# Performance work log

Hardware: AMD Instinct MI355X
Metric: run time of the kernel (lower is better)

Reference implementation:

```python
import jax, jax.numpy as jnp
import numpy as np

N_NODES = 100000
N_EDGES = 1000000
IN_CH = 128
HID = 128


def setup_inputs() -> dict:
    key = jax.random.key(0)
    ks = jax.random.split(key, 8)
    node_features = jax.random.normal(ks[0], (N_NODES, IN_CH), dtype=jnp.float32)
    edge_index = jax.random.randint(ks[1], (2, N_EDGES), 0, N_NODES, dtype=jnp.int64)
    # Linear params (PyTorch convention: W [out,in], y = x @ W.T + b), Kaiming-ish scale
    Wdim = jax.random.normal(ks[2], (HID, IN_CH), dtype=jnp.float32) / np.sqrt(IN_CH)
    bdim = jnp.zeros((HID,), dtype=jnp.float32)
    W1 = jax.random.normal(ks[3], (HID, 2 * HID), dtype=jnp.float32) / np.sqrt(2 * HID)
    b1 = jnp.zeros((HID,), dtype=jnp.float32)
    W2 = jax.random.normal(ks[4], (1, HID), dtype=jnp.float32) / np.sqrt(HID)
    b2 = jnp.zeros((1,), dtype=jnp.float32)
    return {"node_features": node_features, "edge_index": edge_index,
            "Wdim": Wdim, "bdim": bdim, "W1": W1, "b1": b1, "W2": W2, "b2": b2}


def reference(node_features, edge_index, Wdim, bdim, W1, b1, W2, b2):
    # gather endpoint features [E, in_ch]
    src = node_features[edge_index[0]]
    dst = node_features[edge_index[1]]
    # shared first projection + ReLU (dropout = identity at eval)
    x = jax.nn.relu(src @ Wdim.T + bdim)  # [E, H]
    y = jax.nn.relu(dst @ Wdim.T + bdim)  # [E, H]
    # elementwise combine -> [E, 2H]
    edge_feat = jnp.concatenate([x * y, x - y], axis=1)
    h = jax.nn.relu(edge_feat @ W1.T + b1)  # [E, H]
    prob = jax.nn.sigmoid(h @ W2.T + b2)  # [E, 1]
    return prob
```

## Files before the change

### kernel.cpp

```cpp
#include <hip/hip_runtime.h>
#include <hip/hip_bf16.h>


#define N_NODES 100000
#define N_EDGES 1000000
#define NT      31250
#define GRID    1024

typedef unsigned int u32;
typedef u32   u32x2 __attribute__((ext_vector_type(2)));
typedef u32   u32x4 __attribute__((ext_vector_type(4)));
typedef float f32x4 __attribute__((ext_vector_type(4)));
typedef float f32x16 __attribute__((ext_vector_type(16)));
typedef __bf16 bf16x8 __attribute__((ext_vector_type(8)));
typedef _Float16 f16x8 __attribute__((ext_vector_type(8)));

__device__ inline u32 pack2bf(float a, float b) {
    unsigned short ua = __builtin_bit_cast(unsigned short, (__bf16)a);
    unsigned short ub = __builtin_bit_cast(unsigned short, (__bf16)b);
    return (u32)ua | ((u32)ub << 16);
}
__device__ inline u32 pack2h(float a, float b) {
    unsigned short ua = __builtin_bit_cast(unsigned short, (_Float16)a);
    unsigned short ub = __builtin_bit_cast(unsigned short, (_Float16)b);
    return (u32)ua | ((u32)ub << 16);
}

__device__ __forceinline__ void gload16(const unsigned char* g, unsigned char* l) {
    __builtin_amdgcn_global_load_lds(
        (__attribute__((address_space(1))) unsigned int*)g,
        (__attribute__((address_space(3))) unsigned int*)l,
        16, 0, 0);
}

__global__ __launch_bounds__(256, 1) void k_project(
    const float* __restrict__ nf, const float* __restrict__ Wdim,
    const float* __restrict__ bdim, unsigned short* __restrict__ P)
{
    __shared__ unsigned char lA[128 * 256];
    const int t = threadIdx.x;
    for (int ci = t; ci < 2048; ci += 256) {
        const int row = ci >> 4;
        const int k8 = (ci & 15) << 3;
        const float* wp = Wdim + (row << 7) + k8;
        f32x4 v0 = *(const f32x4*)wp;
        f32x4 v1 = *(const f32x4*)(wp + 4);
        u32x4 pk = { pack2bf(v0[0], v0[1]), pack2bf(v0[2], v0[3]),
                     pack2bf(v1[0], v1[1]), pack2bf(v1[2], v1[3]) };
        int byte = (row << 8) + (k8 << 1);
        byte ^= (row & 15) << 4;
        *(u32x4*)(lA + byte) = pk;
    }
    __syncthreads();

    const int lane = t & 63;
    const int wave = t >> 6;
    const int cc = lane & 31;
    const int h  = lane >> 5;
    const int tile = blockIdx.x * 4 + wave;
    if (tile >= 3125) return;
    const int node = (tile << 5) + cc;
    const float* xrow = nf + ((size_t)node << 7);

    f32x4 rv[16];
#pragma unroll
    for (int kt = 0; kt < 8; ++kt) {
        const int kf = (kt << 4) + (h << 3);
        rv[2*kt]   = *(const f32x4*)(xrow + kf);
        rv[2*kt+1] = *(const f32x4*)(xrow + kf + 4);
    }

    f32x16 acc[4] = {};
#pragma unroll
    for (int kt = 0; kt < 8; ++kt) {
        const int kf = (kt << 4) + (h << 3);
        f32x4 v0 = rv[2*kt], v1 = rv[2*kt+1];
        bf16x8 bf;
        bf[0]=(__bf16)v0[0]; bf[1]=(__bf16)v0[1]; bf[2]=(__bf16)v0[2]; bf[3]=(__bf16)v0[3];
        bf[4]=(__bf16)v1[0]; bf[5]=(__bf16)v1[1]; bf[6]=(__bf16)v1[2]; bf[7]=(__bf16)v1[3];
        const int off = kf << 1;
#pragma unroll
        for (int t4 = 0; t4 < 4; ++t4) {
            const int arow = (t4 << 5) + cc;
            const int ab = ((arow << 8) + off) ^ ((arow & 15) << 4);
            bf16x8 af = __builtin_bit_cast(bf16x8, *(const u32x4*)(lA + ab));
            acc[t4] = __builtin_amdgcn_mfma_f32_32x32x16_bf16(af, bf, acc[t4], 0, 0, 0);
        }
    }
    unsigned short* prow = P + ((size_t)node << 7);
#pragma unroll
    for (int t4 = 0; t4 < 4; ++t4) {
#pragma unroll
        for (int q = 0; q < 4; ++q) {
            const int chb = (t4 << 5) + (q << 3) + (h << 2);
            f32x4 bb = *(const f32x4*)(bdim + chb);
            const float h0 = fmaxf(acc[t4][(q << 2) + 0] + bb[0], 0.f);
            const float h1 = fmaxf(acc[t4][(q << 2) + 1] + bb[1], 0.f);
            const float h2 = fmaxf(acc[t4][(q << 2) + 2] + bb[2], 0.f);
            const float h3 = fmaxf(acc[t4][(q << 2) + 3] + bb[3], 0.f);
            u32x2 st = { pack2h(h0, h1), pack2h(h2, h3) };
            *(u32x2*)(prow + chb) = st;
        }
    }
}

__global__ __launch_bounds__(256, 2) void k_edge(
    const unsigned short* __restrict__ P,
    const int* __restrict__ ei,
    const float* __restrict__ W1, const float* __restrict__ b1,
    const float* __restrict__ W2, const float* __restrict__ b2,
    float* __restrict__ out)
{
    __shared__ unsigned char buf[2][64 * 256];
    __shared__ float pr[2][4][32];
    __shared__ float sb1[128], sw2[128];
    const int t = threadIdx.x;
    const int lane = t & 63;
    const int wave = t >> 6;
    const int cc = lane & 31;
    const int h  = lane >> 5;
    if (t < 128) { sb1[t] = b1[t]; sw2[t] = W2[t]; }

    f16x8 wf[16];
    {
        const float* wrow = W1 + (((wave << 5) + cc) << 8);
#pragma unroll
        for (int kt = 0; kt < 8; ++kt) {
#pragma unroll
            for (int half = 0; half < 2; ++half) {
                const float* wp = wrow + (half << 7) + (kt << 4) + (h << 3);
                f32x4 a = *(const f32x4*)wp;
                f32x4 b = *(const f32x4*)(wp + 4);
                f16x8 f;
                f[0]=(_Float16)a[0]; f[1]=(_Float16)a[1]; f[2]=(_Float16)a[2]; f[3]=(_Float16)a[3];
                f[4]=(_Float16)b[0]; f[5]=(_Float16)b[1]; f[6]=(_Float16)b[2]; f[7]=(_Float16)b[3];
                wf[(kt << 1) + half] = f;
            }
        }
    }

    const unsigned char* Pb = (const unsigned char*)P;
    const int* eb = ei + (wave < 2 ? 0 : N_EDGES - 32);
    int xo[4], rbase[4];
#pragma unroll
    for (int i = 0; i < 4; ++i) {
        const int rl = (i << 2) + (lane >> 4);
        xo[i] = ((lane & 15) ^ (rl & 15)) << 4;
        rbase[i] = (wave << 4) + rl;
    }
    const float b2v = b2[0];
    const int t0 = blockIdx.x;

    int nidx0, nidx1, nidx2, nidx3;
    {
        int i0 = eb[(t0 << 5) + rbase[0]];
        int i1 = eb[(t0 << 5) + rbase[1]];
        int i2 = eb[(t0 << 5) + rbase[2]];
        int i3 = eb[(t0 << 5) + rbase[3]];
        gload16(Pb + ((size_t)i0 << 8) + xo[0], &buf[0][(rbase[0] & ~3) << 8]);
        gload16(Pb + ((size_t)i1 << 8) + xo[1], &buf[0][(rbase[1] & ~3) << 8]);
        gload16(Pb + ((size_t)i2 << 8) + xo[2], &buf[0][(rbase[2] & ~3) << 8]);
        gload16(Pb + ((size_t)i3 << 8) + xo[3], &buf[0][(rbase[3] & ~3) << 8]);
        int tn = t0 + GRID; tn = tn < NT ? tn : NT - 1;
        nidx0 = eb[(tn << 5) + rbase[0]];
        nidx1 = eb[(tn << 5) + rbase[1]];
        nidx2 = eb[(tn << 5) + rbase[2]];
        nidx3 = eb[(tn << 5) + rbase[3]];
    }
    __syncthreads();

    int p = 0;
    for (int tl = t0; tl < NT; tl += GRID) {
        unsigned char* nb = buf[p ^ 1];
        gload16(Pb + ((size_t)nidx0 << 8) + xo[0], nb + ((rbase[0] & ~3) << 8));
        gload16(Pb + ((size_t)nidx1 << 8) + xo[1], nb + ((rbase[1] & ~3) << 8));
        gload16(Pb + ((size_t)nidx2 << 8) + xo[2], nb + ((rbase[2] & ~3) << 8));
        gload16(Pb + ((size_t)nidx3 << 8) + xo[3], nb + ((rbase[3] & ~3) << 8));
        {
            int tn = tl + 2 * GRID; tn = tn < NT ? tn : NT - 1;
            nidx0 = eb[(tn << 5) + rbase[0]];
            nidx1 = eb[(tn << 5) + rbase[1]];
            nidx2 = eb[(tn << 5) + rbase[2]];
            nidx3 = eb[(tn << 5) + rbase[3]];
        }

        const unsigned char* bp_ = buf[p];
        const unsigned char* xb = bp_ + (cc << 8);
        const unsigned char* yb = bp_ + ((32 + cc) << 8);
        const int cx = cc & 15;
        f32x16 acc = {};
#pragma unroll
        for (int kt = 0; kt < 8; ++kt) {
            const int co = (((kt << 1) + h) ^ cx) << 4;
            const f16x8 xh = __builtin_bit_cast(f16x8, *(const u32x4*)(xb + co));
            const f16x8 yh = __builtin_bit_cast(f16x8, *(const u32x4*)(yb + co));
            const f16x8 bp = xh * yh;
            const f16x8 bd = xh - yh;
            acc = __builtin_amdgcn_mfma_f32_32x32x16_f16(wf[(kt << 1) + 0], bp, acc, 0, 0, 0);
            acc = __builtin_amdgcn_mfma_f32_32x32x16_f16(wf[(kt << 1) + 1], bd, acc, 0, 0, 0);
        }

        float partial = 0.f;
#pragma unroll
        for (int q = 0; q < 4; ++q) {
            const int chb = (wave << 5) + (q << 3) + (h << 2);
            const f32x4 bb = *(const f32x4*)(sb1 + chb);
            const f32x4 ww = *(const f32x4*)(sw2 + chb);
#pragma unroll
            for (int rr = 0; rr < 4; ++rr) {
                const float hv = fmaxf(acc[(q << 2) + rr] + bb[rr], 0.f);
                partial += hv * ww[rr];
            }
        }
        partial += __shfl_xor(partial, 32);
        if (h == 0) pr[p][wave][cc] = partial;

        __syncthreads();

        if (t < 32) {
            const float z = pr[p][0][t] + pr[p][1][t] + pr[p][2][t] + pr[p][3][t] + b2v;
            out[(tl << 5) + t] = 1.0f / (1.0f + __expf(-z));
        }
        p ^= 1;
    }
}

extern "C" void kernel_launch(void* const* d_in, const int* in_sizes, int n_in,
                              void* d_out, int out_size, void* d_ws, size_t ws_size,
                              hipStream_t stream) {
    const float* nf   = (const float*)d_in[0];
    const int*   ei   = (const int*)d_in[1];
    const float* Wdim = (const float*)d_in[2];
    const float* bdim = (const float*)d_in[3];
    const float* W1   = (const float*)d_in[4];
    const float* b1   = (const float*)d_in[5];
    const float* W2   = (const float*)d_in[6];
    const float* b2   = (const float*)d_in[7];
    float* out = (float*)d_out;
    unsigned short* P = (unsigned short*)d_ws;

    k_project<<<dim3(782), dim3(256), 0, stream>>>(nf, Wdim, bdim, P);
    k_edge<<<dim3(GRID), dim3(256), 0, stream>>>(P, ei, W1, b1, W2, b2, out);
}
```

Baseline: 150.6 us.

## Triple-buffer edge gathers with explicit waitcnt and deferred output writes

Replaces the double-buffered LDS gather pipeline in the edge kernel with a three-stage ring of buffers, prefetching gathered node rows two tiles ahead. A manual s_waitcnt vmcnt plus s_barrier replaces __syncthreads, and each tile's sigmoid output is written in the following iteration, which removes one barrier per tile. The grid drops from 1024 to 768 blocks to fit the extra LDS buffer. The intent is to hide gather latency better, at the cost of more LDS per block and reliance on hand-counted vmcnt values, which could be fragile.

```diff
diff --git a/kernel.cpp b/kernel.cpp
--- a/kernel.cpp
+++ b/kernel.cpp
@@ -5,7 +5,7 @@
 #define N_NODES 100000
 #define N_EDGES 1000000
 #define NT      31250
-#define GRID    1024
+#define GRID    768
 
 typedef unsigned int u32;
 typedef u32   u32x2 __attribute__((ext_vector_type(2)));
@@ -107,11 +107,13 @@
 __global__ __launch_bounds__(256, 2) void k_edge(
     const unsigned short* __restrict__ P,
     const int* __restrict__ ei,
-    const float* __restrict__ W1, const float* __restrict__ b1,
-    const float* __restrict__ W2, const float* __restrict__ b2,
+    const float* __restrict__ W1, const float* __restrict__ B1,
+    const float* __restrict__ W2, const float* __restrict__ B2,
     float* __restrict__ out)
 {
-    __shared__ unsigned char buf[2][64 * 256];
+    __shared__ unsigned char b0[64 * 256];
+    __shared__ unsigned char b1[64 * 256];
+    __shared__ unsigned char b2[64 * 256];
     __shared__ float pr[2][4][32];
     __shared__ float sb1[128], sw2[128];
     const int t = threadIdx.x;
@@ -119,7 +121,7 @@
     const int wave = t >> 6;
     const int cc = lane & 31;
     const int h  = lane >> 5;
-    if (t < 128) { sb1[t] = b1[t]; sw2[t] = W2[t]; }
+    if (t < 128) { sb1[t] = B1[t]; sw2[t] = W2[t]; }
 
     f16x8 wf[16];
     {
@@ -141,87 +143,109 @@
 
     const unsigned char* Pb = (const unsigned char*)P;
     const int* eb = ei + (wave < 2 ? 0 : N_EDGES - 32);
-    int xo[4], rbase[4];
-#pragma unroll
-    for (int i = 0; i < 4; ++i) {
-        const int rl = (i << 2) + (lane >> 4);
-        xo[i] = ((lane & 15) ^ (rl & 15)) << 4;
-        rbase[i] = (wave << 4) + rl;
-    }
-    const float b2v = b2[0];
+    const int rl = lane >> 4;
+    const int rb0 = (wave << 4) + 0  + rl, rb1 = (wave << 4) + 4  + rl;
+    const int rb2 = (wave << 4) + 8  + rl, rb3 = (wave << 4) + 12 + rl;
+    const int xo0 = ((lane & 15) ^ (rb0 & 15)) << 4;
+    const int xo1 = ((lane & 15) ^ (rb1 & 15)) << 4;
+    const int xo2 = ((lane & 15) ^ (rb2 & 15)) << 4;
+    const int xo3 = ((lane & 15) ^ (rb3 & 15)) << 4;
+    const int lbo0 = (rb0 & ~3) << 8, lbo1 = (rb1 & ~3) << 8;
+    const int lbo2 = (rb2 & ~3) << 8, lbo3 = (rb3 & ~3) << 8;
+    const int cx = cc & 15;
+    const float b2v = B2[0];
     const int t0 = blockIdx.x;
 
+    int tl = t0, prev = -1, ph = 0;
     int nidx0, nidx1, nidx2, nidx3;
-    {
-        int i0 = eb[(t0 << 5) + rbase[0]];
-        int i1 = eb[(t0 << 5) + rbase[1]];
-        int i2 = eb[(t0 << 5) + rbase[2]];
-        int i3 = eb[(t0 << 5) + rbase[3]];
-        gload16(Pb + ((size_t)i0 << 8) + xo[0], &buf[0][(rbase[0] & ~3) << 8]);
-        gload16(Pb + ((size_t)i1 << 8) + xo[1], &buf[0][(rbase[1] & ~3) << 8]);
-        gload16(Pb + ((size_t)i2 << 8) + xo[2], &buf[0][(rbase[2] & ~3) << 8]);
-        gload16(Pb + ((size_t)i3 << 8) + xo[3], &buf[0][(rbase[3] & ~3) << 8]);
+
+    {
+        const int* e0 = eb + (t0 << 5);
+        int i0 = e0[rb0], i1 = e0[rb1], i2 = e0[rb2], i3 = e0[rb3];
+        gload16(Pb + ((size_t)i0 << 8) + xo0, b0 + lbo0);
+        gload16(Pb + ((size_t)i1 << 8) + xo1, b0 + lbo1);
+        gload16(Pb + ((size_t)i2 << 8) + xo2, b0 + lbo2);
+        gload16(Pb + ((size_t)i3 << 8) + xo3, b0 + lbo3);
+    }
+    {
         int tn = t0 + GRID; tn = tn < NT ? tn : NT - 1;
-        nidx0 = eb[(tn << 5) + rbase[0]];
-        nidx1 = eb[(tn << 5) + rbase[1]];
-        nidx2 = eb[(tn << 5) + rbase[2]];
-        nidx3 = eb[(tn << 5) + rbase[3]];
+        const int* e1 = eb + (tn << 5);
+        int i0 = e1[rb0], i1 = e1[rb1], i2 = e1[rb2], i3 = e1[rb3];
+        gload16(Pb + ((size_t)i0 << 8) + xo0, b1 + lbo0);
+        gload16(Pb + ((size_t)i1 << 8) + xo1, b1 + lbo1);
+        gload16(Pb + ((size_t)i2 << 8) + xo2, b1 + lbo2);
+        gload16(Pb + ((size_t)i3 << 8) + xo3, b1 + lbo3);
+    }
+    {
+        int tn = t0 + 2 * GRID; tn = tn < NT ? tn : NT - 1;
+        const int* e2 = eb + (tn << 5);
+        nidx0 = e2[rb0]; nidx1 = e2[rb1]; nidx2 = e2[rb2]; nidx3 = e2[rb3];
     }
     __syncthreads();
 
-    int p = 0;
-    for (int tl = t0; tl < NT; tl += GRID) {
-        unsigned char* nb = buf[p ^ 1];
-        gload16(Pb + ((size_t)nidx0 << 8) + xo[0], nb + ((rbase[0] & ~3) << 8));
-        gload16(Pb + ((size_t)nidx1 << 8) + xo[1], nb + ((rbase[1] & ~3) << 8));
-        gload16(Pb + ((size_t)nidx2 << 8) + xo[2], nb + ((rbase[2] & ~3) << 8));
-        gload16(Pb + ((size_t)nidx3 << 8) + xo[3], nb + ((rbase[3] & ~3) << 8));
-        {
-            int tn = tl + 2 * GRID; tn = tn < NT ? tn : NT - 1;
-            nidx0 = eb[(tn << 5) + rbase[0]];
-            nidx1 = eb[(tn << 5) + rbase[1]];
-            nidx2 = eb[(tn << 5) + rbase[2]];
-            nidx3 = eb[(tn << 5) + rbase[3]];
-        }
-
-        const unsigned char* bp_ = buf[p];
-        const unsigned char* xb = bp_ + (cc << 8);
-        const unsigned char* yb = bp_ + ((32 + cc) << 8);
-        const int cx = cc & 15;
-        f32x16 acc = {};
-#pragma unroll
-        for (int kt = 0; kt < 8; ++kt) {
-            const int co = (((kt << 1) + h) ^ cx) << 4;
-            const f16x8 xh = __builtin_bit_cast(f16x8, *(const u32x4*)(xb + co));
-            const f16x8 yh = __builtin_bit_cast(f16x8, *(const u32x4*)(yb + co));
-            const f16x8 bp = xh * yh;
-            const f16x8 bd = xh - yh;
-            acc = __builtin_amdgcn_mfma_f32_32x32x16_f16(wf[(kt << 1) + 0], bp, acc, 0, 0, 0);
-            acc = __builtin_amdgcn_mfma_f32_32x32x16_f16(wf[(kt << 1) + 1], bd, acc, 0, 0, 0);
-        }
-
-        float partial = 0.f;
-#pragma unroll
-        for (int q = 0; q < 4; ++q) {
-            const int chb = (wave << 5) + (q << 3) + (h << 2);
-            const f32x4 bb = *(const f32x4*)(sb1 + chb);
-            const f32x4 ww = *(const f32x4*)(sw2 + chb);
-#pragma unroll
-            for (int rr = 0; rr < 4; ++rr) {
-                const float hv = fmaxf(acc[(q << 2) + rr] + bb[rr], 0.f);
-                partial += hv * ww[rr];
-            }
-        }
-        partial += __shfl_xor(partial, 32);
-        if (h == 0) pr[p][wave][cc] = partial;
-
-        __syncthreads();
-
-        if (t < 32) {
-            const float z = pr[p][0][t] + pr[p][1][t] + pr[p][2][t] + pr[p][3][t] + b2v;
-            out[(tl << 5) + t] = 1.0f / (1.0f + __expf(-z));
-        }
-        p ^= 1;
+#define STEP(BC, BS)                                                          \
+    {                                                                         \
+        asm volatile("s_waitcnt vmcnt(8)\n\ts_barrier" ::: "memory");         \
+        if (prev >= 0 && t < 32) {                                            \
+            const int pp = ph ^ 1;                                            \
+            const float z = pr[pp][0][t] + pr[pp][1][t] + pr[pp][2][t]        \
+                          + pr[pp][3][t] + b2v;                               \
+            out[(prev << 5) + t] = 1.0f / (1.0f + __expf(-z));                \
+        }                                                                     \
+        gload16(Pb + ((size_t)nidx0 << 8) + xo0, (BS) + lbo0);                \
+        gload16(Pb + ((size_t)nidx1 << 8) + xo1, (BS) + lbo1);                \
+        gload16(Pb + ((size_t)nidx2 << 8) + xo2, (BS) + lbo2);                \
+        gload16(Pb + ((size_t)nidx3 << 8) + xo3, (BS) + lbo3);                \
+        {   int tn = tl + 3 * GRID; tn = tn < NT ? tn : NT - 1;               \
+            const int* ebn = eb + (tn << 5);                                  \
+            nidx0 = ebn[rb0]; nidx1 = ebn[rb1];                               \
+            nidx2 = ebn[rb2]; nidx3 = ebn[rb3]; }                             \
+        const unsigned char* xb = (BC) + (cc << 8);                           \
+        const unsigned char* yb = (BC) + ((32 + cc) << 8);                    \
+        f32x16 acc = {};                                                      \
+        _Pragma("unroll")                                                     \
+        for (int kt = 0; kt < 8; ++kt) {                                      \
+            const int co = (((kt << 1) + h) ^ cx) << 4;                       \
+            const f16x8 xh = __builtin_bit_cast(f16x8, *(const u32x4*)(xb + co)); \
+            const f16x8 yh = __builtin_bit_cast(f16x8, *(const u32x4*)(yb + co)); \
+            const f16x8 bpv = xh * yh;                                        \
+            const f16x8 bdv = xh - yh;                                        \
+            acc = __builtin_amdgcn_mfma_f32_32x32x16_f16(wf[(kt << 1) + 0], bpv, acc, 0, 0, 0); \
+            acc = __builtin_amdgcn_mfma_f32_32x32x16_f16(wf[(kt << 1) + 1], bdv, acc, 0, 0, 0); \
+        }                                                                     \
+        float partial = 0.f;                                                  \
+        _Pragma("unroll")                                                     \
+        for (int q = 0; q < 4; ++q) {                                         \
+            const int chb = (wave << 5) + (q << 3) + (h << 2);                \
+            const f32x4 bb = *(const f32x4*)(sb1 + chb);                      \
+            const f32x4 ww = *(const f32x4*)(sw2 + chb);                      \
+            _Pragma("unroll")                                                 \
+            for (int rr = 0; rr < 4; ++rr) {                                  \
+                const float hv = fmaxf(acc[(q << 2) + rr] + bb[rr], 0.f);     \
+                partial += hv * ww[rr];                                       \
+            }                                                                 \
+        }                                                                     \
+        partial += __shfl_xor(partial, 32);                                   \
+        if (h == 0) pr[ph][wave][cc] = partial;                               \
+        asm volatile("s_waitcnt lgkmcnt(0)" ::: "memory");                    \
+        prev = tl; tl += GRID; ph ^= 1;                                       \
+    }
+
+    while (tl < NT) {
+        STEP(b0, b2);
+        if (tl >= NT) break;
+        STEP(b1, b0);
+        if (tl >= NT) break;
+        STEP(b2, b1);
+    }
+#undef STEP
+
+    asm volatile("s_barrier" ::: "memory");
+    if (prev >= 0 && t < 32) {
+        const int pp = ph ^ 1;
+        const float z = pr[pp][0][t] + pr[pp][1][t] + pr[pp][2][t]
+                      + pr[pp][3][t] + b2v;
+        out[(prev << 5) + t] = 1.0f / (1.0f + __expf(-z));
     }
 }
 
```

Measured after the change: 132.0 us. 1.14x faster.
